# Kernel tuning notes

Measured on AMD Instinct MI355X. Metric: run time of the kernel, lower is better.

## Reference

```python
import jax, jax.numpy as jnp
import numpy as np

PI = 3.1415926
MAX_V = 8  # max vertices of a quad-quad convex intersection
ALPHA, GAMMA, IOU_THRES = 0.25, 2.0, 0.5


def xyxy2xywh_a(b):
    cx = (b[..., 0] + b[..., 2]) * 0.5
    cy = (b[..., 1] + b[..., 3]) * 0.5
    w = b[..., 2] - b[..., 0]
    h = b[..., 3] - b[..., 1]
    return jnp.stack([cx, cy, w, h, b[..., 4]], -1)


def rbox_2_quad(b):
    # [N,5] (x1,y1,x2,y2,theta_deg) -> [N,4,2] corner quads
    x = xyxy2xywh_a(b)
    cx, cy, w, h, t = x[:, 0], x[:, 1], x[:, 2], x[:, 3], x[:, 4]
    th = t * (PI / 180.0)
    c, s = jnp.cos(th), jnp.sin(th)
    dx = jnp.array([-0.5, 0.5, 0.5, -0.5], b.dtype)
    dy = jnp.array([-0.5, -0.5, 0.5, 0.5], b.dtype)
    px = cx[:, None] + dx * w[:, None] * c[:, None] - dy * h[:, None] * s[:, None]
    py = cy[:, None] + dx * w[:, None] * s[:, None] + dy * h[:, None] * c[:, None]
    return jnp.stack([px, py], -1)


def min_area_square(b):
    cx = (b[:, 0] + b[:, 2]) * 0.5
    cy = (b[:, 1] + b[:, 3]) * 0.5
    s = jnp.maximum(b[:, 2] - b[:, 0], b[:, 3] - b[:, 1]) * 0.5
    return jnp.stack([cx - s, cy - s, cx + s, cy + s], 1)


def bbox_overlaps(a, b):
    # axis-aligned IoU matrix [N,M]
    lt = jnp.maximum(a[:, None, :2], b[None, :, :2])
    rb = jnp.minimum(a[:, None, 2:], b[None, :, 2:])
    wh = jnp.clip(rb - lt, 0.0)
    inter = wh[..., 0] * wh[..., 1]
    area_a = (a[:, 2] - a[:, 0]) * (a[:, 3] - a[:, 1])
    area_b = (b[:, 2] - b[:, 0]) * (b[:, 3] - b[:, 1])
    return inter / (area_a[:, None] + area_b[None, :] - inter + 1e-6)


def points_in_quads(pts, quads):
    # pointsJf: pts [A,2] inside convex quads [G,4,2] -> [A,G] {0,1}
    e = jnp.roll(quads, -1, axis=1) - quads  # [G,4,2]
    rel = pts[:, None, None, :] - quads[None]  # [A,G,4,2]
    cr = e[None, ..., 0] * rel[..., 1] - e[None, ..., 1] * rel[..., 0]
    inside = jnp.all(cr >= 0, -1) | jnp.all(cr <= 0, -1)
    return inside.astype(pts.dtype)


def _signed_area2(q):
    return jnp.sum(q[:, 0] * jnp.roll(q[:, 1], -1) - jnp.roll(q[:, 0], -1) * q[:, 1])


def _quad_inter_area(q1, q2):
    # Sutherland-Hodgman clipping of quad q1 by convex quad q2, fixed 8-vertex buffer
    q1 = jnp.where(_signed_area2(q1) < 0, q1[::-1], q1)
    q2 = jnp.where(_signed_area2(q2) < 0, q2[::-1], q2)
    poly = jnp.zeros((MAX_V, 2), q1.dtype).at[:4].set(q1)
    edges = jnp.stack([q2, jnp.roll(q2, -1, axis=0)], 1)  # [4,2,2]

    def clip(carry, edge):
        poly, n = carry
        a, b = edge[0], edge[1]
        idx = jnp.arange(MAX_V)
        nidx = jnp.where(idx + 1 < n, idx + 1, 0)
        cur, nxt = poly, poly[nidx]
        d = b - a
        dc = d[0] * (cur[:, 1] - a[1]) - d[1] * (cur[:, 0] - a[0])
        dn = d[0] * (nxt[:, 1] - a[1]) - d[1] * (nxt[:, 0] - a[0])
        denom = dc - dn
        t = dc / jnp.where(jnp.abs(denom) < 1e-12, 1e-12, denom)
        inter = cur + t[:, None] * (nxt - cur)
        active = idx < n
        keep_cur = active & (dc >= 0)
        keep_int = active & ((dc >= 0) != (dn >= 0))
        pts = jnp.stack([cur, inter], 1).reshape(2 * MAX_V, 2)
        flags = jnp.stack([keep_cur, keep_int], 1).reshape(-1)
        pos = jnp.where(flags, jnp.cumsum(flags) - 1, MAX_V)
        newpoly = jnp.zeros((MAX_V + 1, 2), poly.dtype).at[pos].set(pts)[:MAX_V]
        return (newpoly, flags.sum()), None

    (poly, n), _ = jax.lax.scan(clip, (poly, jnp.int32(4)), edges)
    idx = jnp.arange(MAX_V)
    nidx = jnp.where(idx + 1 < n, idx + 1, 0)
    contrib = poly[:, 0] * poly[nidx, 1] - poly[nidx, 0] * poly[:, 1]
    area = 0.5 * jnp.abs(jnp.sum(jnp.where(idx < n, contrib, 0.0)))
    return jnp.where(n >= 3, area, 0.0)


def rbox_overlaps(quads_a, quads_g, gate, thresh=0.1):
    area_a = 0.5 * jnp.abs(jax.vmap(_signed_area2)(quads_a))
    area_g = 0.5 * jnp.abs(jax.vmap(_signed_area2)(quads_g))
    inter = jax.vmap(lambda qa: jax.vmap(lambda qg: _quad_inter_area(qa, qg))(quads_g))(quads_a)
    iou = inter / (area_a[:, None] + area_g[None, :] - inter + 1e-6)
    return jnp.where(gate > thresh, iou, 0.0)


def encode(anchors, gt):
    a = xyxy2xywh_a(anchors)
    g = xyxy2xywh_a(gt)
    dx = (g[:, 0] - a[:, 0]) / a[:, 2]
    dy = (g[:, 1] - a[:, 1]) / a[:, 3]
    dw = jnp.log(g[:, 2] / a[:, 2])
    dh = jnp.log(g[:, 3] / a[:, 3])
    dt = (g[:, 4] - a[:, 4]) * (PI / 180.0)
    return jnp.stack([dx, dy, dw, dh, dt], 1)


def decode(anchors, deltas):
    a = xyxy2xywh_a(anchors)
    cx = a[..., 0] + deltas[..., 0] * a[..., 2]
    cy = a[..., 1] + deltas[..., 1] * a[..., 3]
    w = a[..., 2] * jnp.exp(deltas[..., 2])
    h = a[..., 3] * jnp.exp(deltas[..., 3])
    t = a[..., 4] + deltas[..., 4] * (180.0 / PI)
    return jnp.stack([cx, cy, w, h, t], -1)


def smooth_l1(x, t, beta=1.0 / 9):
    diff = jnp.abs(x - t)
    return jnp.where(diff < beta, 0.5 * diff * diff / beta, diff - 0.5 * beta)


def _forward(classifications, regressions, anchors, annotations):
    B = classifications.shape[0]
    _ = decode(anchors, regressions)  # all_pred_boxes (unused when func='smooth')
    cls_losses, reg_losses = [], []
    for j in range(B):
        cls = jnp.clip(classifications[j], 1e-4, 1.0 - 1e-4)
        anch = anchors[j]
        gtb = annotations[j, :, :5]
        labels = annotations[j, :, 5].astype(jnp.int32)
        indicator = bbox_overlaps(min_area_square(anch), min_area_square(gtb))
        centers = xyxy2xywh_a(anch)[:, :2]
        quads_g = rbox_2_quad(gtb)
        inside = points_in_quads(centers, quads_g)
        quads_a = rbox_2_quad(anch)
        ious = rbox_overlaps(quads_a, quads_g, inside * indicator)  # [A,G]
        iou_max = ious.max(1)
        iou_argmax = ious.argmax(1)
        pos = iou_max >= IOU_THRES
        max_gt = ious.max(0)
        argmax_gt = ious.argmax(0)
        low = (max_gt < IOU_THRES).astype(jnp.int32)
        pos = (pos.astype(jnp.int32).at[argmax_gt].max(low)).astype(bool)
        num_pos = pos.sum()
        C = cls.shape[1]
        onehot = jax.nn.one_hot(labels[iou_argmax], C, dtype=cls.dtype)
        tgt = -jnp.ones_like(cls)
        tgt = jnp.where((iou_max < IOU_THRES - 0.1)[:, None], 0.0, tgt)
        tgt = jnp.where(pos[:, None], onehot, tgt)
        af = jnp.where(tgt == 1.0, ALPHA, 1.0 - ALPHA)
        fw = af * jnp.where(tgt == 1.0, 1.0 - cls, cls) ** GAMMA
        bce = -(tgt * jnp.log(cls + 1e-6) + (1.0 - tgt) * jnp.log(1.0 - cls + 1e-6))
        cls_loss = jnp.where(tgt != -1.0, fw * bce, 0.0).sum() / jnp.maximum(num_pos.astype(cls.dtype), 1.0)
        cls_losses.append(cls_loss)
        reg_t = encode(anch, gtb[iou_argmax])
        l = smooth_l1(regressions[j], reg_t)
        denom = (jnp.maximum(num_pos, 1) * l.shape[1]).astype(l.dtype)
        reg_loss = jnp.where(num_pos > 0, (l * pos[:, None].astype(l.dtype)).sum() / denom, 0.0)
        reg_losses.append(reg_loss)
    loss_cls = 5.0 * jnp.stack(cls_losses).mean(keepdims=True)
    loss_reg = 2.0 * jnp.stack(reg_losses).mean(keepdims=True)
    return loss_cls, loss_reg


def setup_inputs() -> dict:
    key = jax.random.key(0)
    ks = jax.random.split(key, 8)
    B, A, G, C = 2, 32768, 32, 15
    cls = jax.random.uniform(ks[0], (B, A, C), jnp.float32)
    reg = jax.random.normal(ks[1], (B, A, 5), jnp.float32) * 0.1
    ac = jax.random.uniform(ks[2], (B, A, 2), jnp.float32, 0.0, 1024.0)
    awh = jax.random.uniform(ks[3], (B, A, 2), jnp.float32, 16.0, 256.0)
    anchors = jnp.concatenate([ac - awh * 0.5, ac + awh * 0.5, jnp.zeros((B, A, 1), jnp.float32)], -1)
    gc = jax.random.uniform(ks[4], (B, G, 2), jnp.float32, 64.0, 960.0)
    gwh = jax.random.uniform(ks[5], (B, G, 2), jnp.float32, 24.0, 300.0)
    gt = jax.random.uniform(ks[6], (B, G, 1), jnp.float32, -90.0, 90.0)
    glab = jax.random.randint(ks[7], (B, G, 1), 0, C).astype(jnp.float32)
    annotations = jnp.concatenate([gc - gwh * 0.5, gc + gwh * 0.5, gt, glab], -1)
    return {"classifications": cls, "regressions": reg, "anchors": anchors, "annotations": annotations}


def reference(classifications, regressions, anchors, annotations):
    return _forward(classifications, regressions, anchors, annotations)
```

## Files before the change

### kernel.cpp

```cpp
#include <hip/hip_runtime.h>

#define A_N 32768
#define G_N 32
#define C_N 15
#define APB 64
#define TPB 256
#define H_N 4
#define BPB (A_N / APB)
#define DEG2RAD ((float)(3.1415926 / 180.0))
#define BETA (1.0f / 9.0f)

typedef unsigned long long ull;

template <int NIN>
__device__ __forceinline__ int clip_pass(float ax, float ay, float dx, float dy,
                                         float (&PX)[8], float (&PY)[8], int n) {
  constexpr int NOUT = (NIN + 1 < 8) ? NIN + 1 : 8;
  float d[NIN];
#pragma unroll
  for (int i = 0; i < NIN; ++i)
    d[i] = dx * (PY[i] - ay) - dy * (PX[i] - ax);
  float NX[NOUT], NY[NOUT];
#pragma unroll
  for (int i = 0; i < NOUT; ++i) { NX[i] = 0.f; NY[i] = 0.f; }
  int m = 0;
#pragma unroll
  for (int i = 0; i < NIN; ++i) {
    if (i < n) {
      bool w = (i + 1 < n);
      float dn = w ? d[(i + 1) % NIN] : d[0];
      float xn = w ? PX[(i + 1) % NIN] : PX[0];
      float yn = w ? PY[(i + 1) % NIN] : PY[0];
      bool kc = (d[i] >= 0.f);
      bool kn = (dn >= 0.f);
      if (kc) {
#pragma unroll
        for (int o = 0; o < NOUT; ++o)
          if (o <= 2 * i && m == o) { NX[o] = PX[i]; NY[o] = PY[i]; }
        ++m;
      }
      if (kc != kn) {
        float den = d[i] - dn;
        if (fabsf(den) < 1e-12f) den = 1e-12f;
        float t = d[i] / den;
        float ix = PX[i] + t * (xn - PX[i]);
        float iy = PY[i] + t * (yn - PY[i]);
#pragma unroll
        for (int o = 0; o < NOUT; ++o)
          if (o <= 2 * i + 1 && m == o) { NX[o] = ix; NY[o] = iy; }
        ++m;
      }
    }
  }
#pragma unroll
  for (int i = 0; i < NOUT; ++i) { PX[i] = NX[i]; PY[i] = NY[i]; }
#pragma unroll
  for (int i = NOUT; i < 8; ++i) { PX[i] = 0.f; PY[i] = 0.f; }
  return m;
}

__global__ __launch_bounds__(TPB, 4) void k_fused(
    const float* __restrict__ cls_in, const float* __restrict__ reg_in,
    const float* __restrict__ anchors, const float* __restrict__ annot,
    ull* __restrict__ gpart, ull* __restrict__ rowpack,
    float* __restrict__ cls_part, float* __restrict__ reg_part,
    int* __restrict__ cnt_part) {
  int j = blockIdx.x >> 9;
  int blk = blockIdx.x & (BPB - 1);
  int tid = threadIdx.x;
  int la = tid & (APB - 1);
  int h = tid >> 6;
  int a = blk * APB + la;
  size_t ia = (size_t)j * A_N + a;

  __shared__ float4 g_sqv[G_N];
  __shared__ float2 g_meta[G_N];
  __shared__ float4 g_vx[G_N], g_vy[G_N];
  __shared__ float4 a_qx[APB], a_qy[APB];
  __shared__ float a_area[APB];
  __shared__ ull rowbest[APB];
  __shared__ ull colmax[G_N];
  __shared__ unsigned short list[APB * G_N];
  __shared__ int cnt;
  __shared__ int lab[G_N];
  __shared__ float gcx[G_N], gcy[G_N], gw2[G_N], gh2[G_N], gth[G_N];
  __shared__ float w1[H_N], w2[H_N];
  __shared__ int w3[H_N];

  float pcv[4];
  {
    const float* c = cls_in + ia * C_N;
#pragma unroll
    for (int k = 0; k < 4; ++k) {
      int ci = h * 4 + k;
      pcv[k] = (ci < C_N) ? c[ci] : 0.f;
    }
  }
  float rvv[5];
  if (h == 0) {
    const float* r = reg_in + ia * 5;
#pragma unroll
    for (int i = 0; i < 5; ++i) rvv[i] = r[i];
  } else {
#pragma unroll
    for (int i = 0; i < 5; ++i) rvv[i] = 0.f;
  }

  if (tid == 0) cnt = 0;
  if (tid < APB) rowbest[tid] = 0xFFFFFFFFull;
  if (tid < G_N) colmax[tid] = 0xFFFFFFFFull;

  if (tid < G_N) {
    const float* g = annot + ((size_t)j * G_N + tid) * 6;
    float x1 = g[0], y1 = g[1], x2 = g[2], y2 = g[3], t = g[4];
    float cxx = (x1 + x2) * 0.5f, cyy = (y1 + y2) * 0.5f;
    float w = x2 - x1, hh = y2 - y1;
    gcx[tid] = cxx; gcy[tid] = cyy; gw2[tid] = w; gh2[tid] = hh; gth[tid] = t;
    lab[tid] = (int)g[5];
    float th = t * DEG2RAD;
    float c = __cosf(th), s = __sinf(th);
    const float ddx[4] = {-0.5f, 0.5f, 0.5f, -0.5f};
    const float ddy[4] = {-0.5f, -0.5f, 0.5f, 0.5f};
    float px[4], py[4];
#pragma unroll
    for (int k = 0; k < 4; ++k) {
      px[k] = cxx + ddx[k] * w * c - ddy[k] * hh * s;
      py[k] = cyy + ddx[k] * w * s + ddy[k] * hh * c;
    }
    float s2 = 0.f;
#pragma unroll
    for (int k = 0; k < 4; ++k)
      s2 += px[k] * py[(k + 1) & 3] - px[(k + 1) & 3] * py[k];
    if (s2 < 0.f) {
      g_vx[tid] = make_float4(px[3], px[2], px[1], px[0]);
      g_vy[tid] = make_float4(py[3], py[2], py[1], py[0]);
    } else {
      g_vx[tid] = make_float4(px[0], px[1], px[2], px[3]);
      g_vy[tid] = make_float4(py[0], py[1], py[2], py[3]);
    }
    float half = fmaxf(w, hh) * 0.5f;
    float sx1 = cxx - half, sy1 = cyy - half, sx2 = cxx + half, sy2 = cyy + half;
    g_sqv[tid] = make_float4(sx1, sy1, sx2, sy2);
    g_meta[tid] = make_float2((sx2 - sx1) * (sy2 - sy1), 0.5f * fabsf(s2));
  }

  const float* an = anchors + ia * 5;
  float ax1 = an[0], ay1 = an[1], ax2 = an[2], ay2 = an[3], at = an[4];
  float acx = (ax1 + ax2) * 0.5f, acy = (ay1 + ay2) * 0.5f;
  float aw = ax2 - ax1, ah = ay2 - ay1;
  float ath = at * DEG2RAD;
  float ac = __cosf(ath), asn = __sinf(ath);
  {
    const float ddx[4] = {-0.5f, 0.5f, 0.5f, -0.5f};
    const float ddy[4] = {-0.5f, -0.5f, 0.5f, 0.5f};
    float apx[4], apy[4];
#pragma unroll
    for (int k = 0; k < 4; ++k) {
      apx[k] = acx + ddx[k] * aw * ac - ddy[k] * ah * asn;
      apy[k] = acy + ddx[k] * aw * asn + ddy[k] * ah * ac;
    }
    float s2a = 0.f;
#pragma unroll
    for (int k = 0; k < 4; ++k)
      s2a += apx[k] * apy[(k + 1) & 3] - apx[(k + 1) & 3] * apy[k];
    if (s2a < 0.f) {
      float tx = apx[0], ty = apy[0];
      apx[0] = apx[3]; apy[0] = apy[3]; apx[3] = tx; apy[3] = ty;
      tx = apx[1]; ty = apy[1];
      apx[1] = apx[2]; apy[1] = apy[2]; apx[2] = tx; apy[2] = ty;
    }
    if (h == 0) {
      a_qx[la] = make_float4(apx[0], apx[1], apx[2], apx[3]);
      a_qy[la] = make_float4(apy[0], apy[1], apy[2], apy[3]);
      a_area[la] = 0.5f * fabsf(s2a);
    }
  }
  float half = fmaxf(aw, ah) * 0.5f;
  float asx1 = acx - half, asy1 = acy - half, asx2 = acx + half, asy2 = acy + half;
  float asarea = (asx2 - asx1) * (asy2 - asy1);
  __syncthreads();

#pragma unroll
  for (int gg = 0; gg < G_N / H_N; ++gg) {
    int g = h * (G_N / H_N) + gg;
    float4 sq = g_sqv[g];
    float2 meta = g_meta[g];
    float ltx = fmaxf(asx1, sq.x);
    float lty = fmaxf(asy1, sq.y);
    float rbx = fminf(asx2, sq.z);
    float rby = fminf(asy2, sq.w);
    float iw = fmaxf(rbx - ltx, 0.f);
    float ih = fmaxf(rby - lty, 0.f);
    float inter_s = iw * ih;
    float ind = inter_s / (asarea + meta.x - inter_s + 1e-6f);
    float4 vx = g_vx[g], vy = g_vy[g];
    float cr0 = (vx.y - vx.x) * (acy - vy.x) - (vy.y - vy.x) * (acx - vx.x);
    float cr1 = (vx.z - vx.y) * (acy - vy.y) - (vy.z - vy.y) * (acx - vx.y);
    float cr2 = (vx.w - vx.z) * (acy - vy.z) - (vy.w - vy.z) * (acx - vx.z);
    float cr3 = (vx.x - vx.w) * (acy - vy.w) - (vy.x - vy.w) * (acx - vx.w);
    bool pall = (cr0 >= 0.f) & (cr1 >= 0.f) & (cr2 >= 0.f) & (cr3 >= 0.f);
    bool nall = (cr0 <= 0.f) & (cr1 <= 0.f) & (cr2 <= 0.f) & (cr3 <= 0.f);
    if ((pall || nall) && ind > 0.1f) {
      int p = atomicAdd(&cnt, 1);
      list[p] = (unsigned short)((la << 5) | g);
    }
  }
  __syncthreads();

  int np = cnt;
  for (int i = tid; i < np; i += TPB) {
    int ent = list[i];
    int ca = ent >> 5, g = ent & 31;
    float4 aqx = a_qx[ca], aqy = a_qy[ca];
    float PX[8], PY[8];
    PX[0] = aqx.x; PX[1] = aqx.y; PX[2] = aqx.z; PX[3] = aqx.w;
    PY[0] = aqy.x; PY[1] = aqy.y; PY[2] = aqy.z; PY[3] = aqy.w;
#pragma unroll
    for (int k = 4; k < 8; ++k) { PX[k] = 0.f; PY[k] = 0.f; }
    float4 gvx = g_vx[g], gvy = g_vy[g];
    int n = 4;
    n = clip_pass<4>(gvx.x, gvy.x, gvx.y - gvx.x, gvy.y - gvy.x, PX, PY, n);
    n = clip_pass<5>(gvx.y, gvy.y, gvx.z - gvx.y, gvy.z - gvy.y, PX, PY, n);
    n = clip_pass<6>(gvx.z, gvy.z, gvx.w - gvx.z, gvy.w - gvy.z, PX, PY, n);
    n = clip_pass<7>(gvx.w, gvy.w, gvx.x - gvx.w, gvy.x - gvy.w, PX, PY, n);
    float s = 0.f;
#pragma unroll
    for (int k = 0; k < 8; ++k) {
      if (k < n) {
        float xn = (k + 1 < n) ? PX[(k + 1) & 7] : PX[0];
        float yn = (k + 1 < n) ? PY[(k + 1) & 7] : PY[0];
        s += PX[k] * yn - xn * PY[k];
      }
    }
    float inter = (n >= 3) ? 0.5f * fabsf(s) : 0.f;
    float v = inter / (a_area[ca] + g_meta[g].y - inter + 1e-6f);
    ull pr = ((ull)__float_as_uint(v) << 32) | (unsigned)(~(unsigned)g);
    atomicMax(&rowbest[ca], pr);
    unsigned ga = (unsigned)(blk * APB + ca);
    ull pc = ((ull)__float_as_uint(v) << 32) | (unsigned)(~ga);
    atomicMax(&colmax[g], pc);
  }
  __syncthreads();

  ull rb = rowbest[la];
  float im = __uint_as_float((unsigned)(rb >> 32));
  int arg = (int)(~(unsigned)rb);
  int p = (im >= 0.5f) ? 1 : 0;

  if (h == 0) rowpack[ia] = rb;
  if (tid < G_N)
    gpart[((size_t)j * BPB + blk) * G_N + tid] = colmax[tid];

  int lb = lab[arg];
  float csum = 0.f;
  bool bg = (im < 0.4f);
  if (p || bg) {
#pragma unroll
    for (int k = 0; k < 4; ++k) {
      int ci = h * 4 + k;
      if (ci < C_N) {
        float pc = fminf(fmaxf(pcv[k], 1e-4f), 0.9999f);
        bool tgt1 = p && (ci == lb);
        if (tgt1)
          csum += 0.25f * (1.f - pc) * (1.f - pc) * (-__logf(pc + 1e-6f));
        else
          csum += 0.75f * pc * pc * (-__logf(1.f - pc + 1e-6f));
      }
    }
  }

  float rsum = 0.f;
  if (p && h == 0) {
    float t5[5];
    t5[0] = (gcx[arg] - acx) / aw;
    t5[1] = (gcy[arg] - acy) / ah;
    t5[2] = __logf(gw2[arg] / aw);
    t5[3] = __logf(gh2[arg] / ah);
    t5[4] = (gth[arg] - at) * DEG2RAD;
#pragma unroll
    for (int i = 0; i < 5; ++i) {
      float d = fabsf(rvv[i] - t5[i]);
      rsum += (d < BETA) ? (0.5f * d * d / BETA) : (d - 0.5f * BETA);
    }
  }
  int pcnt = (h == 0) ? p : 0;

  float v1 = csum, v2 = rsum;
  int v3 = pcnt;
#pragma unroll
  for (int off = 32; off; off >>= 1) {
    v1 += __shfl_xor(v1, off);
    v2 += __shfl_xor(v2, off);
    v3 += __shfl_xor(v3, off);
  }
  int ln = tid & 63;
  if (ln == 0) { w1[h] = v1; w2[h] = v2; w3[h] = v3; }
  __syncthreads();
  if (tid == 0) {
    cls_part[blockIdx.x] = (w1[0] + w1[1]) + (w1[2] + w1[3]);
    reg_part[blockIdx.x] = (w2[0] + w2[1]) + (w2[2] + w2[3]);
    cnt_part[blockIdx.x] = (w3[0] + w3[1]) + (w3[2] + w3[3]);
  }
}

__global__ __launch_bounds__(256) void k_fix(
    const float* __restrict__ cls_in, const float* __restrict__ reg_in,
    const float* __restrict__ anchors, const float* __restrict__ annot,
    const ull* __restrict__ gpart, const ull* __restrict__ rowpack,
    const float* __restrict__ cls_part, const float* __restrict__ reg_part,
    const int* __restrict__ cnt_part, float* __restrict__ out, int B) {
  int tid = threadIdx.x;
  __shared__ ull sred[8][G_N];
  __shared__ int fanchor[G_N];
  __shared__ float dcs[G_N], drs[G_N];
  __shared__ int dct[G_N];
  __shared__ float bd_c[8], bd_r[8];
  __shared__ int bd_n[8];
  __shared__ float s1[256], s2[256];
  __shared__ int s3[256];

  for (int j = 0; j < B; ++j) {
    {
      int g = tid & 31, chunk = tid >> 5;
      const ull* gp = gpart + (size_t)j * BPB * G_N;
      ull m = 0;
      for (int b = 0; b < BPB / 8; ++b) {
        ull v = gp[(size_t)(chunk * (BPB / 8) + b) * G_N + g];
        m = v > m ? v : m;
      }
      sred[chunk][g] = m;
    }
    __syncthreads();
    if (tid < G_N) {
      ull m = sred[0][tid];
#pragma unroll
      for (int c = 1; c < 8; ++c) m = sred[c][tid] > m ? sred[c][tid] : m;
      float v = __uint_as_float((unsigned)(m >> 32));
      fanchor[tid] = (v < 0.5f) ? (int)(~(unsigned)m) : -1;
      dcs[tid] = 0.f; drs[tid] = 0.f; dct[tid] = 0;
    }
    __syncthreads();
    if (tid < G_N) {
      int af = fanchor[tid];
      bool owner = (af >= 0);
      for (int g2 = 0; g2 < tid; ++g2)
        owner = owner && (fanchor[g2] != af);
      if (owner) {
        size_t ia = (size_t)j * A_N + af;
        ull rb = rowpack[ia];
        float im = __uint_as_float((unsigned)(rb >> 32));
        if (im < 0.5f) {
          int arg = (int)(~(unsigned)rb);
          const float* gg = annot + ((size_t)j * G_N + arg) * 6;
          int lb = (int)gg[5];
          const float* c = cls_in + ia * C_N;
          bool bg = (im < 0.4f);
          float ca = 0.f, cb = 0.f;
#pragma unroll
          for (int ci = 0; ci < C_N; ++ci) {
            float pc = fminf(fmaxf(c[ci], 1e-4f), 0.9999f);
            float neg = 0.75f * pc * pc * (-__logf(1.f - pc + 1e-6f));
            if (ci == lb)
              ca += 0.25f * (1.f - pc) * (1.f - pc) * (-__logf(pc + 1e-6f));
            else
              ca += neg;
            if (bg) cb += neg;
          }
          const float* an = anchors + ia * 5;
          float acx = (an[0] + an[2]) * 0.5f, acy = (an[1] + an[3]) * 0.5f;
          float aw = an[2] - an[0], ah = an[3] - an[1];
          float gcxv = (gg[0] + gg[2]) * 0.5f, gcyv = (gg[1] + gg[3]) * 0.5f;
          float gwv = gg[2] - gg[0], ghv = gg[3] - gg[1];
          const float* r = reg_in + ia * 5;
          float t5[5];
          t5[0] = (gcxv - acx) / aw;
          t5[1] = (gcyv - acy) / ah;
          t5[2] = __logf(gwv / aw);
          t5[3] = __logf(ghv / ah);
          t5[4] = (gg[4] - an[4]) * DEG2RAD;
          float rs = 0.f;
#pragma unroll
          for (int i = 0; i < 5; ++i) {
            float d = fabsf(r[i] - t5[i]);
            rs += (d < BETA) ? (0.5f * d * d / BETA) : (d - 0.5f * BETA);
          }
          dcs[tid] = ca - cb;
          drs[tid] = rs;
          dct[tid] = 1;
        }
      }
    }
    __syncthreads();
    if (tid == 0) {
      float dc = 0.f, dr = 0.f;
      int dn = 0;
#pragma unroll
      for (int g = 0; g < G_N; ++g) { dc += dcs[g]; dr += drs[g]; dn += dct[g]; }
      bd_c[j] = dc; bd_r[j] = dr; bd_n[j] = dn;
    }
    __syncthreads();
  }

  int P = B * BPB;
  float cv = 0.f, rvv = 0.f;
  int nv = 0;
#pragma unroll
  for (int k = 0; k < 4; ++k) {
    int idx = tid * 4 + k;
    if (idx < P) { cv += cls_part[idx]; rvv += reg_part[idx]; nv += cnt_part[idx]; }
  }
  s1[tid] = cv; s2[tid] = rvv; s3[tid] = nv;
  __syncthreads();
  for (int o = 64; o; o >>= 1) {
    if ((tid & 127) < o) {
      s1[tid] += s1[tid + o]; s2[tid] += s2[tid + o]; s3[tid] += s3[tid + o];
    }
    __syncthreads();
  }
  if (tid == 0) {
    float cl = 0.f, rl = 0.f;
    for (int jj = 0; jj < B; ++jj) {
      float cs = s1[jj * 128] + bd_c[jj];
      float rs = s2[jj * 128] + bd_r[jj];
      int np = s3[jj * 128] + bd_n[jj];
      float npf = (np > 0) ? (float)np : 1.f;
      cl += cs / npf;
      rl += (np > 0) ? rs / (npf * 5.f) : 0.f;
    }
    out[0] = 5.0f * cl / (float)B;
    out[1] = 2.0f * rl / (float)B;
  }
}

extern "C" void kernel_launch(void* const* d_in, const int* in_sizes, int n_in,
                              void* d_out, int out_size, void* d_ws, size_t ws_size,
                              hipStream_t stream) {
  const float* cls = (const float*)d_in[0];
  const float* reg = (const float*)d_in[1];
  const float* anc = (const float*)d_in[2];
  const float* ann = (const float*)d_in[3];
  int B = in_sizes[3] / (G_N * 6);

  char* w = (char*)d_ws;
  ull* gpart = (ull*)w;        w += (size_t)B * BPB * G_N * sizeof(ull);
  ull* rowpack = (ull*)w;      w += (size_t)B * A_N * sizeof(ull);
  float* cls_part = (float*)w; w += (size_t)B * BPB * 4;
  float* reg_part = (float*)w; w += (size_t)B * BPB * 4;
  int* cnt_part = (int*)w;     w += (size_t)B * BPB * 4;

  k_fused<<<B * BPB, TPB, 0, stream>>>(cls, reg, anc, ann, gpart, rowpack,
                                       cls_part, reg_part, cnt_part);
  k_fix<<<1, 256, 0, stream>>>(cls, reg, anc, ann, gpart, rowpack,
                               cls_part, reg_part, cnt_part, (float*)d_out, B);
}
```

Measured before the change: 41.06 us.

## Fuse final reduction into main kernel via last-block pattern, enlarge blocks

Drops the separate single-block fixup kernel and has the last block to finish, detected through an atomic done counter, run the per-GT fix and the final reduction. Blocks grow from 64 to 256 anchors with 1024 threads, which cuts the block count and the number of partials to reduce. Candidate list appends now use a wave ballot with one atomic per wave instead of one atomic per thread. In exchange the launch needs an extra memset, the big blocks may hurt occupancy and register allocation, and the tail work still runs serially on one block.

Result: slower. 47.65 us (+16.0%).

```diff
diff --git a/kernel.cpp b/kernel.cpp
--- a/kernel.cpp
+++ b/kernel.cpp
@@ -3,8 +3,8 @@
 #define A_N 32768
 #define G_N 32
 #define C_N 15
-#define APB 64
-#define TPB 256
+#define APB 256
+#define TPB 1024
 #define H_N 4
 #define BPB (A_N / APB)
 #define DEG2RAD ((float)(3.1415926 / 180.0))
@@ -59,17 +59,18 @@
   return m;
 }
 
-__global__ __launch_bounds__(TPB, 4) void k_fused(
+__global__ __launch_bounds__(TPB) void k_fused(
     const float* __restrict__ cls_in, const float* __restrict__ reg_in,
     const float* __restrict__ anchors, const float* __restrict__ annot,
     ull* __restrict__ gpart, ull* __restrict__ rowpack,
     float* __restrict__ cls_part, float* __restrict__ reg_part,
-    int* __restrict__ cnt_part) {
-  int j = blockIdx.x >> 9;
+    int* __restrict__ cnt_part, unsigned* __restrict__ done,
+    float* __restrict__ out, int B) {
+  int j = blockIdx.x >> 7;
   int blk = blockIdx.x & (BPB - 1);
   int tid = threadIdx.x;
   int la = tid & (APB - 1);
-  int h = tid >> 6;
+  int h = tid >> 8;
   int a = blk * APB + la;
   size_t ia = (size_t)j * A_N + a;
 
@@ -84,8 +85,17 @@
   __shared__ int cnt;
   __shared__ int lab[G_N];
   __shared__ float gcx[G_N], gcy[G_N], gw2[G_N], gh2[G_N], gth[G_N];
-  __shared__ float w1[H_N], w2[H_N];
-  __shared__ int w3[H_N];
+  __shared__ float w1[16], w2[16];
+  __shared__ int w3[16];
+  __shared__ ull sredF[16][G_N];
+  __shared__ int fanchorF[G_N];
+  __shared__ float dcsF[G_N], drsF[G_N];
+  __shared__ int dctF[G_N];
+  __shared__ float bdcF[8], bdrF[8];
+  __shared__ int bdnF[8];
+  __shared__ float s1F[256], s2F[256];
+  __shared__ int s3F[256];
+  __shared__ int amLast;
 
   float pcv[4];
   {
@@ -180,6 +190,7 @@
   float asarea = (asx2 - asx1) * (asy2 - asy1);
   __syncthreads();
 
+  int ln = tid & 63;
 #pragma unroll
   for (int gg = 0; gg < G_N / H_N; ++gg) {
     int g = h * (G_N / H_N) + gg;
@@ -200,9 +211,15 @@
     float cr3 = (vx.x - vx.w) * (acy - vy.w) - (vy.x - vy.w) * (acx - vx.w);
     bool pall = (cr0 >= 0.f) & (cr1 >= 0.f) & (cr2 >= 0.f) & (cr3 >= 0.f);
     bool nall = (cr0 <= 0.f) & (cr1 <= 0.f) & (cr2 <= 0.f) & (cr3 <= 0.f);
-    if ((pall || nall) && ind > 0.1f) {
-      int p = atomicAdd(&cnt, 1);
-      list[p] = (unsigned short)((la << 5) | g);
+    bool surv = (pall || nall) && (ind > 0.1f);
+    ull bal = __ballot(surv);
+    int nsv = __popcll(bal);
+    int base = 0;
+    if (ln == 0 && nsv) base = atomicAdd(&cnt, nsv);
+    base = __shfl(base, 0);
+    if (surv) {
+      int pre = __popcll(bal & ((1ull << ln) - 1ull));
+      list[base + pre] = (unsigned short)((la << 5) | g);
     }
   }
   __syncthreads();
@@ -293,100 +310,95 @@
     v2 += __shfl_xor(v2, off);
     v3 += __shfl_xor(v3, off);
   }
-  int ln = tid & 63;
-  if (ln == 0) { w1[h] = v1; w2[h] = v2; w3[h] = v3; }
+  int wv = tid >> 6;
+  if (ln == 0) { w1[wv] = v1; w2[wv] = v2; w3[wv] = v3; }
   __syncthreads();
   if (tid == 0) {
-    cls_part[blockIdx.x] = (w1[0] + w1[1]) + (w1[2] + w1[3]);
-    reg_part[blockIdx.x] = (w2[0] + w2[1]) + (w2[2] + w2[3]);
-    cnt_part[blockIdx.x] = (w3[0] + w3[1]) + (w3[2] + w3[3]);
-  }
-}
-
-__global__ __launch_bounds__(256) void k_fix(
-    const float* __restrict__ cls_in, const float* __restrict__ reg_in,
-    const float* __restrict__ anchors, const float* __restrict__ annot,
-    const ull* __restrict__ gpart, const ull* __restrict__ rowpack,
-    const float* __restrict__ cls_part, const float* __restrict__ reg_part,
-    const int* __restrict__ cnt_part, float* __restrict__ out, int B) {
-  int tid = threadIdx.x;
-  __shared__ ull sred[8][G_N];
-  __shared__ int fanchor[G_N];
-  __shared__ float dcs[G_N], drs[G_N];
-  __shared__ int dct[G_N];
-  __shared__ float bd_c[8], bd_r[8];
-  __shared__ int bd_n[8];
-  __shared__ float s1[256], s2[256];
-  __shared__ int s3[256];
-
-  for (int j = 0; j < B; ++j) {
-    {
+    float t1 = 0.f, t2 = 0.f;
+    int t3 = 0;
+#pragma unroll
+    for (int k = 0; k < 16; ++k) { t1 += w1[k]; t2 += w2[k]; t3 += w3[k]; }
+    __hip_atomic_store(&cls_part[blockIdx.x], t1, __ATOMIC_RELAXED, __HIP_MEMORY_SCOPE_AGENT);
+    __hip_atomic_store(&reg_part[blockIdx.x], t2, __ATOMIC_RELAXED, __HIP_MEMORY_SCOPE_AGENT);
+    __hip_atomic_store(&cnt_part[blockIdx.x], t3, __ATOMIC_RELAXED, __HIP_MEMORY_SCOPE_AGENT);
+    __threadfence();
+    unsigned old = __hip_atomic_fetch_add(done, 1u, __ATOMIC_ACQ_REL, __HIP_MEMORY_SCOPE_AGENT);
+    amLast = (old == (unsigned)(gridDim.x - 1)) ? 1 : 0;
+  }
+  __syncthreads();
+  if (!amLast) return;
+  __threadfence();
+
+  for (int jj = 0; jj < B; ++jj) {
+    if (tid < 512) {
       int g = tid & 31, chunk = tid >> 5;
-      const ull* gp = gpart + (size_t)j * BPB * G_N;
+      const ull* gp = gpart + (size_t)jj * BPB * G_N;
       ull m = 0;
-      for (int b = 0; b < BPB / 8; ++b) {
-        ull v = gp[(size_t)(chunk * (BPB / 8) + b) * G_N + g];
+#pragma unroll
+      for (int b = 0; b < 8; ++b) {
+        ull v = __hip_atomic_load(&gp[(size_t)(chunk * 8 + b) * G_N + g],
+                                  __ATOMIC_RELAXED, __HIP_MEMORY_SCOPE_AGENT);
         m = v > m ? v : m;
       }
-      sred[chunk][g] = m;
+      sredF[chunk][g] = m;
     }
     __syncthreads();
     if (tid < G_N) {
-      ull m = sred[0][tid];
-#pragma unroll
-      for (int c = 1; c < 8; ++c) m = sred[c][tid] > m ? sred[c][tid] : m;
+      ull m = sredF[0][tid];
+#pragma unroll
+      for (int c = 1; c < 16; ++c) m = sredF[c][tid] > m ? sredF[c][tid] : m;
       float v = __uint_as_float((unsigned)(m >> 32));
-      fanchor[tid] = (v < 0.5f) ? (int)(~(unsigned)m) : -1;
-      dcs[tid] = 0.f; drs[tid] = 0.f; dct[tid] = 0;
+      fanchorF[tid] = (v < 0.5f) ? (int)(~(unsigned)m) : -1;
+      dcsF[tid] = 0.f; drsF[tid] = 0.f; dctF[tid] = 0;
     }
     __syncthreads();
     if (tid < G_N) {
-      int af = fanchor[tid];
+      int af = fanchorF[tid];
       bool owner = (af >= 0);
       for (int g2 = 0; g2 < tid; ++g2)
-        owner = owner && (fanchor[g2] != af);
+        owner = owner && (fanchorF[g2] != af);
       if (owner) {
-        size_t ia = (size_t)j * A_N + af;
-        ull rb = rowpack[ia];
-        float im = __uint_as_float((unsigned)(rb >> 32));
-        if (im < 0.5f) {
-          int arg = (int)(~(unsigned)rb);
-          const float* gg = annot + ((size_t)j * G_N + arg) * 6;
-          int lb = (int)gg[5];
-          const float* c = cls_in + ia * C_N;
-          bool bg = (im < 0.4f);
+        size_t ja = (size_t)jj * A_N + af;
+        ull rbf = __hip_atomic_load(&rowpack[ja], __ATOMIC_RELAXED, __HIP_MEMORY_SCOPE_AGENT);
+        float imf = __uint_as_float((unsigned)(rbf >> 32));
+        if (imf < 0.5f) {
+          int ag = (int)(~(unsigned)rbf);
+          const float* gg = annot + ((size_t)jj * G_N + ag) * 6;
+          int lbf = (int)gg[5];
+          const float* c = cls_in + ja * C_N;
+          bool bgf = (imf < 0.4f);
           float ca = 0.f, cb = 0.f;
 #pragma unroll
           for (int ci = 0; ci < C_N; ++ci) {
             float pc = fminf(fmaxf(c[ci], 1e-4f), 0.9999f);
             float neg = 0.75f * pc * pc * (-__logf(1.f - pc + 1e-6f));
-            if (ci == lb)
+            if (ci == lbf)
               ca += 0.25f * (1.f - pc) * (1.f - pc) * (-__logf(pc + 1e-6f));
             else
               ca += neg;
-            if (bg) cb += neg;
+            if (bgf) cb += neg;
           }
-          const float* an = anchors + ia * 5;
-          float acx = (an[0] + an[2]) * 0.5f, acy = (an[1] + an[3]) * 0.5f;
-          float aw = an[2] - an[0], ah = an[3] - an[1];
+          const float* anf = anchors + ja * 5;
+          float acxf = (anf[0] + anf[2]) * 0.5f, acyf = (anf[1] + anf[3]) * 0.5f;
+          float awf = anf[2] - anf[0], ahf = anf[3] - anf[1];
           float gcxv = (gg[0] + gg[2]) * 0.5f, gcyv = (gg[1] + gg[3]) * 0.5f;
           float gwv = gg[2] - gg[0], ghv = gg[3] - gg[1];
-          const float* r = reg_in + ia * 5;
+          const float* r = reg_in + ja * 5;
           float t5[5];
-          t5[0] = (gcxv - acx) / aw;
-          t5[1] = (gcyv - acy) / ah;
-          t5[2] = __logf(gwv / aw);
-          t5[3] = __logf(ghv / ah);
-          t5[4] = (gg[4] - an[4]) * DEG2RAD;
+          t5[0] = (gcxv - acxf) / awf;
+          t5[1] = (gcyv - acyf) / ahf;
+          t5[2] = __logf(gwv / awf);
+          t5[3] = __logf(ghv / ahf);
+          t5[4] = (gg[4] - anf[4]) * DEG2RAD;
           float rs = 0.f;
 #pragma unroll
           for (int i = 0; i < 5; ++i) {
             float d = fabsf(r[i] - t5[i]);
             rs += (d < BETA) ? (0.5f * d * d / BETA) : (d - 0.5f * BETA);
           }
-          dcs[tid] = ca - cb;
-          drs[tid] = rs;
-          dct[tid] = 1;
+          dcsF[tid] = ca - cb;
+          drsF[tid] = rs;
+          dctF[tid] = 1;
         }
       }
     }
@@ -395,37 +407,39 @@
       float dc = 0.f, dr = 0.f;
       int dn = 0;
 #pragma unroll
-      for (int g = 0; g < G_N; ++g) { dc += dcs[g]; dr += drs[g]; dn += dct[g]; }
-      bd_c[j] = dc; bd_r[j] = dr; bd_n[j] = dn;
+      for (int g = 0; g < G_N; ++g) { dc += dcsF[g]; dr += drsF[g]; dn += dctF[g]; }
+      bdcF[jj] = dc; bdrF[jj] = dr; bdnF[jj] = dn;
     }
     __syncthreads();
   }
 
   int P = B * BPB;
-  float cv = 0.f, rvv = 0.f;
-  int nv = 0;
-#pragma unroll
-  for (int k = 0; k < 4; ++k) {
-    int idx = tid * 4 + k;
-    if (idx < P) { cv += cls_part[idx]; rvv += reg_part[idx]; nv += cnt_part[idx]; }
-  }
-  s1[tid] = cv; s2[tid] = rvv; s3[tid] = nv;
+  if (tid < 256) {
+    float cv = 0.f, rv2 = 0.f;
+    int nv = 0;
+    if (tid < P) {
+      cv = __hip_atomic_load(&cls_part[tid], __ATOMIC_RELAXED, __HIP_MEMORY_SCOPE_AGENT);
+      rv2 = __hip_atomic_load(&reg_part[tid], __ATOMIC_RELAXED, __HIP_MEMORY_SCOPE_AGENT);
+      nv = __hip_atomic_load(&cnt_part[tid], __ATOMIC_RELAXED, __HIP_MEMORY_SCOPE_AGENT);
+    }
+    s1F[tid] = cv; s2F[tid] = rv2; s3F[tid] = nv;
+  }
   __syncthreads();
   for (int o = 64; o; o >>= 1) {
-    if ((tid & 127) < o) {
-      s1[tid] += s1[tid + o]; s2[tid] += s2[tid + o]; s3[tid] += s3[tid + o];
+    if (tid < 256 && (tid & 127) < o) {
+      s1F[tid] += s1F[tid + o]; s2F[tid] += s2F[tid + o]; s3F[tid] += s3F[tid + o];
     }
     __syncthreads();
   }
   if (tid == 0) {
     float cl = 0.f, rl = 0.f;
     for (int jj = 0; jj < B; ++jj) {
-      float cs = s1[jj * 128] + bd_c[jj];
-      float rs = s2[jj * 128] + bd_r[jj];
-      int np = s3[jj * 128] + bd_n[jj];
-      float npf = (np > 0) ? (float)np : 1.f;
+      float cs = s1F[jj * 128] + bdcF[jj];
+      float rs = s2F[jj * 128] + bdrF[jj];
+      int npn = s3F[jj * 128] + bdnF[jj];
+      float npf = (npn > 0) ? (float)npn : 1.f;
       cl += cs / npf;
-      rl += (np > 0) ? rs / (npf * 5.f) : 0.f;
+      rl += (npn > 0) ? rs / (npf * 5.f) : 0.f;
     }
     out[0] = 5.0f * cl / (float)B;
     out[1] = 2.0f * rl / (float)B;
@@ -442,14 +456,15 @@
   int B = in_sizes[3] / (G_N * 6);
 
   char* w = (char*)d_ws;
+  unsigned* done = (unsigned*)w;  w += 64;
   ull* gpart = (ull*)w;        w += (size_t)B * BPB * G_N * sizeof(ull);
   ull* rowpack = (ull*)w;      w += (size_t)B * A_N * sizeof(ull);
   float* cls_part = (float*)w; w += (size_t)B * BPB * 4;
   float* reg_part = (float*)w; w += (size_t)B * BPB * 4;
   int* cnt_part = (int*)w;     w += (size_t)B * BPB * 4;
 
+  hipMemsetAsync(done, 0, sizeof(unsigned), stream);
   k_fused<<<B * BPB, TPB, 0, stream>>>(cls, reg, anc, ann, gpart, rowpack,
-                                       cls_part, reg_part, cnt_part);
-  k_fix<<<1, 256, 0, stream>>>(cls, reg, anc, ann, gpart, rowpack,
-                               cls_part, reg_part, cnt_part, (float*)d_out, B);
+                                       cls_part, reg_part, cnt_part, done,
+                                       (float*)d_out, B);
 }
```
